# Kernel optimization log

Hardware: AMD Instinct MI355X
Metric: run time of the kernel (lower is better)

## Reference

```python
import jax, jax.numpy as jnp
import numpy as np

B, S, H, D = 32, 2048, 1024, 1024  # batch, src seq len, hidden_dim, output_dim


def setup_inputs() -> dict:
    key = jax.random.key(0)
    k1, k2, k3, k4, k5 = jax.random.split(key, 5)
    hidden = jax.random.normal(k1, (B, H), dtype=jnp.float32)
    encoder_outs = jax.random.normal(k2, (B, S, D), dtype=jnp.float32)
    src_lens = jax.random.randint(k3, (B,), 1, S + 1, dtype=jnp.int32)
    src_lens = src_lens.at[0].set(S)  # ensure max(src_lens) == S (matches torch max_len)
    W1 = jax.random.normal(k4, (D, H), dtype=jnp.float32) * (1.0 / np.sqrt(H))
    W2 = jax.random.normal(k5, (D, H + D), dtype=jnp.float32) * (1.0 / np.sqrt(H + D))
    return {"hidden": hidden, "encoder_outs": encoder_outs, "src_lens": src_lens,
            "W1": W1, "W2": W2}


def reference(hidden, encoder_outs, src_lens, W1, W2):
    # x = l1(hidden): [B, D]
    x = hidden @ W1.T
    # unfused QK dot-product: att_score [B, S] (torch keeps it [S, B]; we use batch-first)
    att = jnp.einsum('bsd,bd->bs', encoder_outs, x)
    # length mask [B, S]
    mask = jnp.arange(S, dtype=src_lens.dtype)[None, :] < src_lens[:, None]
    masked = jnp.where(mask, att, 0.0)
    # faithful to original quirk: any exact-zero entry (masked OR genuinely zero score)
    # is replaced with -1e10 before softmax
    masked = jnp.where(masked == 0.0, jnp.float32(-1e10), masked)
    attn = jax.nn.softmax(masked, axis=1)  # softmax over source positions
    # weighted sum of encoder outputs: [B, D]
    ctx = jnp.einsum('bs,bsd->bd', attn, encoder_outs)
    out = jnp.tanh(jnp.concatenate([ctx, hidden], axis=1) @ W2.T)
    # original returns attn_scores with shape [S, B]
    return out, attn.T
```

## Files before the change

kernel.cpp:

```cpp
#include <hip/hip_runtime.h>

namespace {
constexpr int kB = 32;
constexpr int kS = 2048;
constexpr int kH = 1024;
constexpr int kD = 1024;
constexpr int kK2 = kH + kD;
constexpr float kWThresh = 1e-8f;

typedef float f32x4 __attribute__((ext_vector_type(4)));

__device__ inline float waveReduceSum(float v) {
#pragma unroll
  for (int off = 32; off > 0; off >>= 1) v += __shfl_down(v, off, 64);
  return v;
}
__device__ inline float waveReduceMax(float v) {
#pragma unroll
  for (int off = 32; off > 0; off >>= 1) v = fmaxf(v, __shfl_down(v, off, 64));
  return v;
}
}

__global__ __launch_bounds__(256) void k_x(const float* __restrict__ hidden,
                                           const float* __restrict__ W1,
                                           float* __restrict__ x) {
  const int wid = (blockIdx.x * blockDim.x + threadIdx.x) >> 6;
  const int lane = threadIdx.x & 63;
  const int n0 = (wid & 511) * 2;
  const int b0 = (wid >> 9) * 16;
  const float4* w0v = (const float4*)(W1 + (size_t)n0 * kH);
  const float4* w1v = (const float4*)(W1 + (size_t)(n0 + 1) * kH);
  float4 w0[4], w1[4];
#pragma unroll
  for (int i = 0; i < 4; ++i) {
    w0[i] = w0v[lane + 64 * i];
    w1[i] = w1v[lane + 64 * i];
  }
  for (int b = b0; b < b0 + 16; ++b) {
    const float4* hv = (const float4*)(hidden + (size_t)b * kH);
    float a0 = 0.f, a1 = 0.f;
#pragma unroll
    for (int i = 0; i < 4; ++i) {
      const float4 h = hv[lane + 64 * i];
      a0 += w0[i].x * h.x + w0[i].y * h.y + w0[i].z * h.z + w0[i].w * h.w;
      a1 += w1[i].x * h.x + w1[i].y * h.y + w1[i].z * h.z + w1[i].w * h.w;
    }
    a0 = waveReduceSum(a0);
    a1 = waveReduceSum(a1);
    if (lane == 0) {
      x[(size_t)b * kD + n0] = a0;
      x[(size_t)b * kD + n0 + 1] = a1;
    }
  }
}

__global__ __launch_bounds__(256) void k_att(const float* __restrict__ enc,
                                             const float* __restrict__ x,
                                             const int* __restrict__ lens,
                                             float* __restrict__ att) {
  const int lane = threadIdx.x & 63;
  const int wib = threadIdx.x >> 6;
  const int b = blockIdx.x & 31;
  const int s0 = (blockIdx.x >> 5) * 16 + wib * 4;
  const int len = lens[b];
  if (s0 >= len) return;
  const f32x4* xv = (const f32x4*)(x + (size_t)b * kD);
  f32x4 xr[4];
#pragma unroll
  for (int i = 0; i < 4; ++i) xr[i] = xv[lane + 64 * i];
#pragma unroll
  for (int r = 0; r < 4; ++r) {
    const f32x4* ev = (const f32x4*)(enc + ((size_t)b * kS + (s0 + r)) * kD);
    float acc = 0.f;
#pragma unroll
    for (int i = 0; i < 4; ++i) {
      const f32x4 e = __builtin_nontemporal_load(&ev[lane + 64 * i]);
      acc += xr[i].x * e.x + xr[i].y * e.y + xr[i].z * e.z + xr[i].w * e.w;
    }
    acc = waveReduceSum(acc);
    if (lane == 0) att[(size_t)b * kS + s0 + r] = acc;
  }
}

__global__ __launch_bounds__(1024) void k_smctx(const float* __restrict__ att,
                                                const int* __restrict__ lens,
                                                const float* __restrict__ enc,
                                                float* __restrict__ attnT,
                                                float* __restrict__ ctx) {
  const int b = blockIdx.x;
  const int t = threadIdx.x;
  const int len = lens[b];
  __shared__ float sred[16];
  __shared__ float swts[kS];
  __shared__ int sidx[kS];
  __shared__ int scount;

  const float a0 = (t < len) ? att[(size_t)b * kS + t] : 0.0f;
  const float a1 = (t + 1024 < len) ? att[(size_t)b * kS + t + 1024] : 0.0f;
  const float v0 = (a0 == 0.0f) ? -1e10f : a0;
  const float v1 = (a1 == 0.0f) ? -1e10f : a1;

  float m = waveReduceMax(fmaxf(v0, v1));
  if ((t & 63) == 0) sred[t >> 6] = m;
  __syncthreads();
  if (t < 16) {
    float mm = sred[t];
#pragma unroll
    for (int off = 8; off > 0; off >>= 1) mm = fmaxf(mm, __shfl_down(mm, off, 64));
    if (t == 0) sred[0] = mm;
  }
  __syncthreads();
  m = sred[0];
  __syncthreads();

  float p0 = __expf(v0 - m), p1 = __expf(v1 - m);
  float sum = waveReduceSum(p0 + p1);
  if ((t & 63) == 0) sred[t >> 6] = sum;
  __syncthreads();
  if (t < 16) {
    float ss = sred[t];
#pragma unroll
    for (int off = 8; off > 0; off >>= 1) ss += __shfl_down(ss, off, 64);
    if (t == 0) sred[0] = ss;
  }
  __syncthreads();
  const float inv = 1.0f / sred[0];
  p0 *= inv;
  p1 *= inv;

  attnT[(size_t)t * kB + b] = p0;
  attnT[(size_t)(t + 1024) * kB + b] = p1;

  if (t == 0) scount = 0;
  __syncthreads();
  if (p0 > kWThresh) { const int k = atomicAdd(&scount, 1); sidx[k] = t;        swts[k] = p0; }
  if (p1 > kWThresh) { const int k = atomicAdd(&scount, 1); sidx[k] = t + 1024; swts[k] = p1; }
  __syncthreads();

  const int n = scount;
  const float* ebase = enc + (size_t)b * kS * kD + t;
  float acc = 0.f;
  int k = 0;
  for (; k + 4 <= n; k += 4) {
    const float e0 = ebase[(size_t)sidx[k + 0] * kD];
    const float e1 = ebase[(size_t)sidx[k + 1] * kD];
    const float e2 = ebase[(size_t)sidx[k + 2] * kD];
    const float e3 = ebase[(size_t)sidx[k + 3] * kD];
    acc += swts[k + 0] * e0 + swts[k + 1] * e1 + swts[k + 2] * e2 + swts[k + 3] * e3;
  }
  for (; k < n; ++k) acc += swts[k] * ebase[(size_t)sidx[k] * kD];
  ctx[(size_t)b * kD + t] = acc;
}

__global__ __launch_bounds__(256) void k_out(const float* __restrict__ ctx,
                                             const float* __restrict__ hidden,
                                             const float* __restrict__ W2,
                                             float* __restrict__ out) {
  const int wid = (blockIdx.x * blockDim.x + threadIdx.x) >> 6;
  const int lane = threadIdx.x & 63;
  const int n0 = (wid & 511) * 2;
  const int b0 = (wid >> 9) * 16;
  const float4* w0v = (const float4*)(W2 + (size_t)n0 * kK2);
  const float4* w1v = (const float4*)(W2 + (size_t)(n0 + 1) * kK2);
  float4 w0[8], w1[8];
#pragma unroll
  for (int i = 0; i < 8; ++i) {
    w0[i] = w0v[lane + 64 * i];
    w1[i] = w1v[lane + 64 * i];
  }
  for (int b = b0; b < b0 + 16; ++b) {
    const float4* cv = (const float4*)(ctx + (size_t)b * kD);
    const float4* hv = (const float4*)(hidden + (size_t)b * kH);
    float a0 = 0.f, a1 = 0.f;
#pragma unroll
    for (int i = 0; i < 4; ++i) {
      const float4 a = cv[lane + 64 * i];
      a0 += w0[i].x * a.x + w0[i].y * a.y + w0[i].z * a.z + w0[i].w * a.w;
      a1 += w1[i].x * a.x + w1[i].y * a.y + w1[i].z * a.z + w1[i].w * a.w;
    }
#pragma unroll
    for (int i = 0; i < 4; ++i) {
      const float4 h = hv[lane + 64 * i];
      a0 += w0[i + 4].x * h.x + w0[i + 4].y * h.y + w0[i + 4].z * h.z + w0[i + 4].w * h.w;
      a1 += w1[i + 4].x * h.x + w1[i + 4].y * h.y + w1[i + 4].z * h.z + w1[i + 4].w * h.w;
    }
    a0 = waveReduceSum(a0);
    a1 = waveReduceSum(a1);
    if (lane == 0) {
      out[(size_t)b * kD + n0] = tanhf(a0);
      out[(size_t)b * kD + n0 + 1] = tanhf(a1);
    }
  }
}

extern "C" void kernel_launch(void* const* d_in, const int* in_sizes, int n_in,
                              void* d_out, int out_size, void* d_ws, size_t ws_size,
                              hipStream_t stream) {
  const float* hidden = (const float*)d_in[0];
  const float* enc    = (const float*)d_in[1];
  const int*   lens   = (const int*)d_in[2];
  const float* W1     = (const float*)d_in[3];
  const float* W2     = (const float*)d_in[4];

  float* out   = (float*)d_out;
  float* attnT = out + (size_t)kB * kD;

  float* ws  = (float*)d_ws;
  float* att = ws;
  float* x   = ws + 65536;
  float* ctx = ws + 98304;

  k_x<<<256, 256, 0, stream>>>(hidden, W1, x);
  k_att<<<kB * (kS / 16), 256, 0, stream>>>(enc, x, lens, att);
  k_smctx<<<kB, 1024, 0, stream>>>(att, lens, enc, attnT, ctx);
  k_out<<<256, 256, 0, stream>>>(ctx, hidden, W2, out);
}
```

Measured before the change: 67.15 us.

## Precompute hidden half of output GEMV alongside x GEMV; vectorize attention loads

The hidden·W2[:,H:] partial product is moved out of the final kernel into the first GEMV kernel, which now runs twice as many waves covering both W1 and the W2 hidden half. This shortens the critical-path output kernel, which now only multiplies by ctx and adds the precomputed partial before tanh. The attention score kernel issues all 16 encoder loads per wave up front instead of per row and stores four scores with one vector write. It drops the nontemporal hint on the encoder loads, which may change cache behaviour for the later context pass.

```diff
diff --git a/kernel.cpp b/kernel.cpp
--- a/kernel.cpp
+++ b/kernel.cpp
@@ -22,35 +22,39 @@
 }
 }
 
-__global__ __launch_bounds__(256) void k_x(const float* __restrict__ hidden,
-                                           const float* __restrict__ W1,
-                                           float* __restrict__ x) {
-  const int wid = (blockIdx.x * blockDim.x + threadIdx.x) >> 6;
+__global__ __launch_bounds__(256) void k_gemv1(const float* __restrict__ hidden,
+                                               const float* __restrict__ W1,
+                                               const float* __restrict__ W2,
+                                               float* __restrict__ x,
+                                               float* __restrict__ pb) {
+  const int wid_all = blockIdx.x * 4 + (threadIdx.x >> 6);
   const int lane = threadIdx.x & 63;
+  const bool isX = wid_all < 1024;
+  const int wid = wid_all & 1023;
   const int n0 = (wid & 511) * 2;
   const int b0 = (wid >> 9) * 16;
-  const float4* w0v = (const float4*)(W1 + (size_t)n0 * kH);
-  const float4* w1v = (const float4*)(W1 + (size_t)(n0 + 1) * kH);
-  float4 w0[4], w1[4];
-#pragma unroll
-  for (int i = 0; i < 4; ++i) {
-    w0[i] = w0v[lane + 64 * i];
-    w1[i] = w1v[lane + 64 * i];
-  }
+  const float* wbase = isX ? (W1 + (size_t)n0 * kH) : (W2 + (size_t)n0 * kK2 + kH);
+  const size_t wstride = isX ? (size_t)kH : (size_t)kK2;
+  float* dst = isX ? x : pb;
+  const f32x4* w0v = (const f32x4*)(wbase) + lane;
+  const f32x4* w1v = (const f32x4*)(wbase + wstride) + lane;
+  f32x4 w0[4], w1[4];
+#pragma unroll
+  for (int i = 0; i < 4; ++i) { w0[i] = w0v[64 * i]; w1[i] = w1v[64 * i]; }
   for (int b = b0; b < b0 + 16; ++b) {
-    const float4* hv = (const float4*)(hidden + (size_t)b * kH);
-    float a0 = 0.f, a1 = 0.f;
+    const f32x4* hv = (const f32x4*)(hidden + (size_t)b * kH) + lane;
+    f32x4 s0v = {0.f, 0.f, 0.f, 0.f}, s1v = {0.f, 0.f, 0.f, 0.f};
 #pragma unroll
     for (int i = 0; i < 4; ++i) {
-      const float4 h = hv[lane + 64 * i];
-      a0 += w0[i].x * h.x + w0[i].y * h.y + w0[i].z * h.z + w0[i].w * h.w;
-      a1 += w1[i].x * h.x + w1[i].y * h.y + w1[i].z * h.z + w1[i].w * h.w;
-    }
-    a0 = waveReduceSum(a0);
-    a1 = waveReduceSum(a1);
+      const f32x4 h = hv[64 * i];
+      s0v += w0[i] * h;
+      s1v += w1[i] * h;
+    }
+    const float a0 = waveReduceSum(s0v.x + s0v.y + s0v.z + s0v.w);
+    const float a1 = waveReduceSum(s1v.x + s1v.y + s1v.z + s1v.w);
     if (lane == 0) {
-      x[(size_t)b * kD + n0] = a0;
-      x[(size_t)b * kD + n0 + 1] = a1;
+      dst[(size_t)b * kD + n0] = a0;
+      dst[(size_t)b * kD + n0 + 1] = a1;
     }
   }
 }
@@ -65,21 +69,29 @@
   const int s0 = (blockIdx.x >> 5) * 16 + wib * 4;
   const int len = lens[b];
   if (s0 >= len) return;
-  const f32x4* xv = (const f32x4*)(x + (size_t)b * kD);
-  f32x4 xr[4];
-#pragma unroll
-  for (int i = 0; i < 4; ++i) xr[i] = xv[lane + 64 * i];
-#pragma unroll
-  for (int r = 0; r < 4; ++r) {
-    const f32x4* ev = (const f32x4*)(enc + ((size_t)b * kS + (s0 + r)) * kD);
-    float acc = 0.f;
-#pragma unroll
-    for (int i = 0; i < 4; ++i) {
-      const f32x4 e = __builtin_nontemporal_load(&ev[lane + 64 * i]);
-      acc += xr[i].x * e.x + xr[i].y * e.y + xr[i].z * e.z + xr[i].w * e.w;
-    }
-    acc = waveReduceSum(acc);
-    if (lane == 0) att[(size_t)b * kS + s0 + r] = acc;
+  const f32x4* xv = (const f32x4*)(x + (size_t)b * kD) + lane;
+  const f32x4 xr0 = xv[0], xr1 = xv[64], xr2 = xv[128], xr3 = xv[192];
+  const float* eb = enc + ((size_t)b * kS + s0) * kD;
+  const f32x4* r0 = (const f32x4*)(eb) + lane;
+  const f32x4* r1 = (const f32x4*)(eb + kD) + lane;
+  const f32x4* r2 = (const f32x4*)(eb + 2 * kD) + lane;
+  const f32x4* r3 = (const f32x4*)(eb + 3 * kD) + lane;
+  const f32x4 e00 = r0[0], e01 = r0[64], e02 = r0[128], e03 = r0[192];
+  const f32x4 e10 = r1[0], e11 = r1[64], e12 = r1[128], e13 = r1[192];
+  const f32x4 e20 = r2[0], e21 = r2[64], e22 = r2[128], e23 = r2[192];
+  const f32x4 e30 = r3[0], e31 = r3[64], e32 = r3[128], e33 = r3[192];
+  const f32x4 d0 = e00 * xr0 + e01 * xr1 + e02 * xr2 + e03 * xr3;
+  const f32x4 d1 = e10 * xr0 + e11 * xr1 + e12 * xr2 + e13 * xr3;
+  const f32x4 d2 = e20 * xr0 + e21 * xr1 + e22 * xr2 + e23 * xr3;
+  const f32x4 d3 = e30 * xr0 + e31 * xr1 + e32 * xr2 + e33 * xr3;
+  const float a0 = waveReduceSum(d0.x + d0.y + d0.z + d0.w);
+  const float a1 = waveReduceSum(d1.x + d1.y + d1.z + d1.w);
+  const float a2 = waveReduceSum(d2.x + d2.y + d2.z + d2.w);
+  const float a3 = waveReduceSum(d3.x + d3.y + d3.z + d3.w);
+  if (lane == 0) {
+    f32x4 o;
+    o.x = a0; o.y = a1; o.z = a2; o.w = a3;
+    *(f32x4*)(att + (size_t)b * kS + s0) = o;
   }
 }
 
@@ -154,42 +166,32 @@
 }
 
 __global__ __launch_bounds__(256) void k_out(const float* __restrict__ ctx,
-                                             const float* __restrict__ hidden,
+                                             const float* __restrict__ pb,
                                              const float* __restrict__ W2,
                                              float* __restrict__ out) {
   const int wid = (blockIdx.x * blockDim.x + threadIdx.x) >> 6;
   const int lane = threadIdx.x & 63;
   const int n0 = (wid & 511) * 2;
   const int b0 = (wid >> 9) * 16;
-  const float4* w0v = (const float4*)(W2 + (size_t)n0 * kK2);
-  const float4* w1v = (const float4*)(W2 + (size_t)(n0 + 1) * kK2);
-  float4 w0[8], w1[8];
-#pragma unroll
-  for (int i = 0; i < 8; ++i) {
-    w0[i] = w0v[lane + 64 * i];
-    w1[i] = w1v[lane + 64 * i];
-  }
+  const f32x4* w0v = (const f32x4*)(W2 + (size_t)n0 * kK2) + lane;
+  const f32x4* w1v = (const f32x4*)(W2 + (size_t)(n0 + 1) * kK2) + lane;
+  f32x4 w0[4], w1[4];
+#pragma unroll
+  for (int i = 0; i < 4; ++i) { w0[i] = w0v[64 * i]; w1[i] = w1v[64 * i]; }
   for (int b = b0; b < b0 + 16; ++b) {
-    const float4* cv = (const float4*)(ctx + (size_t)b * kD);
-    const float4* hv = (const float4*)(hidden + (size_t)b * kH);
-    float a0 = 0.f, a1 = 0.f;
+    const f32x4* cv = (const f32x4*)(ctx + (size_t)b * kD) + lane;
+    f32x4 s0v = {0.f, 0.f, 0.f, 0.f}, s1v = {0.f, 0.f, 0.f, 0.f};
 #pragma unroll
     for (int i = 0; i < 4; ++i) {
-      const float4 a = cv[lane + 64 * i];
-      a0 += w0[i].x * a.x + w0[i].y * a.y + w0[i].z * a.z + w0[i].w * a.w;
-      a1 += w1[i].x * a.x + w1[i].y * a.y + w1[i].z * a.z + w1[i].w * a.w;
-    }
-#pragma unroll
-    for (int i = 0; i < 4; ++i) {
-      const float4 h = hv[lane + 64 * i];
-      a0 += w0[i + 4].x * h.x + w0[i + 4].y * h.y + w0[i + 4].z * h.z + w0[i + 4].w * h.w;
-      a1 += w1[i + 4].x * h.x + w1[i + 4].y * h.y + w1[i + 4].z * h.z + w1[i + 4].w * h.w;
-    }
-    a0 = waveReduceSum(a0);
-    a1 = waveReduceSum(a1);
+      const f32x4 a = cv[64 * i];
+      s0v += w0[i] * a;
+      s1v += w1[i] * a;
+    }
+    const float a0 = waveReduceSum(s0v.x + s0v.y + s0v.z + s0v.w);
+    const float a1 = waveReduceSum(s1v.x + s1v.y + s1v.z + s1v.w);
     if (lane == 0) {
-      out[(size_t)b * kD + n0] = tanhf(a0);
-      out[(size_t)b * kD + n0 + 1] = tanhf(a1);
+      out[(size_t)b * kD + n0] = tanhf(a0 + pb[(size_t)b * kD + n0]);
+      out[(size_t)b * kD + n0 + 1] = tanhf(a1 + pb[(size_t)b * kD + n0 + 1]);
     }
   }
 }
@@ -207,12 +209,13 @@
   float* attnT = out + (size_t)kB * kD;
 
   float* ws  = (float*)d_ws;
-  float* att = ws;
-  float* x   = ws + 65536;
+  float* x   = ws;
+  float* att = ws + 32768;
   float* ctx = ws + 98304;
-
-  k_x<<<256, 256, 0, stream>>>(hidden, W1, x);
+  float* pb  = ws + 131072;
+
+  k_gemv1<<<512, 256, 0, stream>>>(hidden, W1, W2, x, pb);
   k_att<<<kB * (kS / 16), 256, 0, stream>>>(enc, x, lens, att);
   k_smctx<<<kB, 1024, 0, stream>>>(att, lens, enc, attnT, ctx);
-  k_out<<<256, 256, 0, stream>>>(ctx, hidden, W2, out);
-}
+  k_out<<<256, 256, 0, stream>>>(ctx, pb, W2, out);
+}
```

Result: slower. 74.76 us (+11.3%).
